# Performance work log

Hardware: AMD Instinct MI355X
Metric: run time of the kernel (lower is better)

The kernel has to match this reference:

```python
import jax, jax.numpy as jnp
import numpy as np

NUM_LAYERS = 4
D_MODEL = 512
D_INNER = 1024   # 2 * d_model (Mamba expand=2)
D_STATE = 16
DT_RANK = 32     # ceil(d_model / 16)
D_CONV = 4
BATCH = 2
SEQ = 512
EPS = 1e-5


def _rmsnorm(x, w, eps=EPS):
    # fused add+RMSNorm math: fp32 reduction, scale by weight (no bias)
    x = x.astype(jnp.float32)
    return x * jax.lax.rsqrt(jnp.mean(x * x, axis=-1, keepdims=True) + eps) * w


def _silu(x):
    return x * jax.nn.sigmoid(x)


def _causal_conv(x, w, b):
    # x: (B, D, L); w: (D, K) depthwise causal conv, left-pad K-1, take first L
    xp = jnp.pad(x, ((0, 0), (0, 0), (D_CONV - 1, 0)))
    out = jax.lax.conv_general_dilated(
        xp, w[:, None, :], (1,), 'VALID',
        dimension_numbers=('NCH', 'OIH', 'NCH'),
        feature_group_count=x.shape[1])
    return out + b[None, :, None]


def _selective_scan(u, delta, A, Bm, Cm):
    # u, delta: (B, D, L); A: (D, N); Bm, Cm: (B, N, L)
    xs = (jnp.moveaxis(delta, 2, 0), jnp.moveaxis(u, 2, 0),
          jnp.moveaxis(Bm, 2, 0), jnp.moveaxis(Cm, 2, 0))
    h0 = jnp.zeros((u.shape[0], u.shape[1], A.shape[1]), u.dtype)

    def step(h, xst):
        d_t, u_t, b_t, c_t = xst                     # (B,D),(B,D),(B,N),(B,N)
        dA = jnp.exp(d_t[:, :, None] * A[None])      # (B,D,N) ZOH discretization
        h = h * dA + (d_t * u_t)[:, :, None] * b_t[:, None, :]
        y = jnp.einsum('bdn,bn->bd', h, c_t)
        return h, y

    _, ys = jax.lax.scan(step, h0, xs)
    return jnp.moveaxis(ys, 0, 2)                    # (B, D, L)


def _ssm_branch(x, z, cw, cb, xpw, dtw, dtb, Alog, Dskip):
    x = _silu(_causal_conv(x, cw, cb))                              # (B, Din, L)
    x_dbl = jnp.einsum('rd,bdl->brl', xpw, x)                       # (B, R+2N, L)
    dt, Bm, Cm = jnp.split(x_dbl, [DT_RANK, DT_RANK + D_STATE], axis=1)
    delta = jax.nn.softplus(jnp.einsum('dr,brl->bdl', dtw, dt) + dtb[None, :, None])
    A = -jnp.exp(Alog.astype(jnp.float32))                          # (Din, N)
    y = _selective_scan(x, delta, A, Bm, Cm)
    y = y + Dskip[None, :, None] * x
    return y * _silu(z)


def _encoder(x, norm_w, in_proj_w, convw_f, convb_f, xpw_f, dtw_f, dtb_f,
             Alog_f, Dskip_f, convw_r, convb_r, xpw_r, dtw_r, dtb_r,
             Alog_r, Dskip_r, out_proj_w, normf_w):
    residual = None
    hs = x
    feats = []
    for i in range(NUM_LAYERS):
        # fused add + RMSNorm, prenorm=True, residual_in_fp32
        residual = hs if residual is None else (hs + residual)
        residual = residual.astype(jnp.float32)
        hn = _rmsnorm(residual, norm_w[i])
        # bimamba v2 mixer
        xz = jnp.einsum('ed,bld->bel', in_proj_w[i], hn)            # (B, 2Din, L)
        xi, zi = jnp.split(xz, 2, axis=1)
        y_f = _ssm_branch(xi, zi, convw_f[i], convb_f[i], xpw_f[i], dtw_f[i],
                          dtb_f[i], Alog_f[i], Dskip_f[i])
        y_r = _ssm_branch(xi[:, :, ::-1], zi[:, :, ::-1], convw_r[i], convb_r[i],
                          xpw_r[i], dtw_r[i], dtb_r[i], Alog_r[i], Dskip_r[i])
        y = y_f + y_r[:, :, ::-1]
        hs = jnp.einsum('bel,de->bld', y, out_proj_w[i])
        feats.append(hs)
    out = _rmsnorm(hs + residual, normf_w)                          # prenorm=False
    return out, feats


def setup_inputs() -> dict:
    key = jax.random.key(0)
    ks = jax.random.split(key, 12)
    Ly = NUM_LAYERS
    s = 0.02

    def nrm(k, shape):
        return jax.random.normal(k, shape, jnp.float32) * s

    dt = 1e-3 + jax.random.uniform(ks[11], (Ly, D_INNER), jnp.float32) * (0.1 - 1e-3)
    dtb = jnp.log(jnp.expm1(dt))  # inverse softplus of dt init
    Alog = jnp.log(jnp.broadcast_to(
        jnp.arange(1, D_STATE + 1, dtype=jnp.float32), (Ly, D_INNER, D_STATE)))
    return dict(
        x=jax.random.normal(ks[0], (BATCH, SEQ, D_MODEL), jnp.float32),
        norm_w=jnp.ones((Ly, D_MODEL), jnp.float32),
        in_proj_w=nrm(ks[1], (Ly, 2 * D_INNER, D_MODEL)),
        convw_f=nrm(ks[2], (Ly, D_INNER, D_CONV)),
        convb_f=jnp.zeros((Ly, D_INNER), jnp.float32),
        xpw_f=nrm(ks[3], (Ly, DT_RANK + 2 * D_STATE, D_INNER)),
        dtw_f=nrm(ks[4], (Ly, D_INNER, DT_RANK)),
        dtb_f=dtb,
        Alog_f=Alog,
        Dskip_f=jnp.ones((Ly, D_INNER), jnp.float32),
        convw_r=nrm(ks[5], (Ly, D_INNER, D_CONV)),
        convb_r=jnp.zeros((Ly, D_INNER), jnp.float32),
        xpw_r=nrm(ks[6], (Ly, DT_RANK + 2 * D_STATE, D_INNER)),
        dtw_r=nrm(ks[7], (Ly, D_INNER, DT_RANK)),
        dtb_r=dtb,
        Alog_r=Alog,
        Dskip_r=jnp.ones((Ly, D_INNER), jnp.float32),
        out_proj_w=nrm(ks[8], (Ly, D_MODEL, D_INNER)),
        normf_w=jnp.ones((D_MODEL,), jnp.float32),
    )


def reference(x, norm_w, in_proj_w, convw_f, convb_f, xpw_f, dtw_f, dtb_f,
              Alog_f, Dskip_f, convw_r, convb_r, xpw_r, dtw_r, dtb_r,
              Alog_r, Dskip_r, out_proj_w, normf_w):
    out, feats = _encoder(x, norm_w, in_proj_w, convw_f, convb_f, xpw_f, dtw_f,
                          dtb_f, Alog_f, Dskip_f, convw_r, convb_r, xpw_r,
                          dtw_r, dtb_r, Alog_r, Dskip_r, out_proj_w, normf_w)
    return (out, jnp.stack(feats))
```

## Files before the change

kernel.cpp:

```cpp
#include <hip/hip_runtime.h>

#define BATCH 2
#define SEQ 512
#define DMODEL 512
#define DINNER 1024
#define DSTATE 16
#define DTRANK 32
#define NBL (BATCH*SEQ)
#define EPSV 1e-5f

typedef __attribute__((ext_vector_type(8))) short bf16x8;
typedef __attribute__((ext_vector_type(4))) float f32x4;

static __device__ __forceinline__ float sigmoidf_(float x) {
  return 1.0f / (1.0f + __expf(-x));
}
static __device__ __forceinline__ float softplusf_(float x) {
  return fmaxf(x, 0.0f) + log1pf(__expf(-fabsf(x)));
}
static __device__ __forceinline__ unsigned short f2bf(float x) {
  unsigned int u = __float_as_uint(x);
  unsigned int r = (u + 0x7FFFu + ((u >> 16) & 1u)) >> 16;
  return (unsigned short)r;
}

__global__ __launch_bounds__(256) void wconvert_kernel(
    const float* __restrict__ s0, const float* __restrict__ s1,
    const float* __restrict__ s2, const float* __restrict__ s3,
    const float* __restrict__ s4, const float* __restrict__ s5,
    unsigned short* __restrict__ d0, unsigned short* __restrict__ d1,
    unsigned short* __restrict__ d2, unsigned short* __restrict__ d3,
    unsigned short* __restrict__ d4, unsigned short* __restrict__ d5) {
  long i = (long)(blockIdx.x * 256 + threadIdx.x) * 8;
  const float* src; unsigned short* dst;
  if (i < 4194304)      { src = s0; dst = d0; }
  else if (i < 6291456) { src = s1; dst = d1; i -= 4194304; }
  else if (i < 6553600) { src = s2; dst = d2; i -= 6291456; }
  else if (i < 6815744) { src = s3; dst = d3; i -= 6553600; }
  else if (i < 6946816) { src = s4; dst = d4; i -= 6815744; }
  else                  { src = s5; dst = d5; i -= 6946816; }
  const float4 v0 = *(const float4*)&src[i];
  const float4 v1 = *(const float4*)&src[i + 4];
  bf16x8 o;
  o[0] = (short)f2bf(v0.x); o[1] = (short)f2bf(v0.y);
  o[2] = (short)f2bf(v0.z); o[3] = (short)f2bf(v0.w);
  o[4] = (short)f2bf(v1.x); o[5] = (short)f2bf(v1.y);
  o[6] = (short)f2bf(v1.z); o[7] = (short)f2bf(v1.w);
  *(bf16x8*)&dst[i] = o;
}

__global__ __launch_bounds__(256) void addnorm_kernel(
    const float* __restrict__ hs, float* __restrict__ residual,
    const float* __restrict__ w, float* __restrict__ out,
    unsigned short* __restrict__ outb, int first) {
  const int row = blockIdx.x;
  const int t = threadIdx.x;
  const float* hp = hs + (long)row * DMODEL;
  float* rp = residual + (long)row * DMODEL;
  float r0 = hp[t], r1 = hp[t + 256];
  if (!first) { r0 += rp[t]; r1 += rp[t + 256]; }
  rp[t] = r0; rp[t + 256] = r1;
  float ss = r0 * r0 + r1 * r1;
  #pragma unroll
  for (int off = 32; off; off >>= 1) ss += __shfl_xor(ss, off, 64);
  __shared__ float sw[4];
  const int wid = t >> 6, lane = t & 63;
  if (lane == 0) sw[wid] = ss;
  __syncthreads();
  const float tot = sw[0] + sw[1] + sw[2] + sw[3];
  const float scale = rsqrtf(tot * (1.0f / (float)DMODEL) + EPSV);
  const float v0 = r0 * scale * w[t];
  const float v1 = r1 * scale * w[t + 256];
  if (out) {
    out[(long)row * DMODEL + t] = v0;
    out[(long)row * DMODEL + t + 256] = v1;
  }
  if (outb) {
    outb[(long)row * DMODEL + t] = f2bf(v0);
    outb[(long)row * DMODEL + t + 256] = f2bf(v1);
  }
}

#define LDK 40
#define LDK2 72

__global__ __launch_bounds__(256) void gemm_in_kernel(
    const unsigned short* __restrict__ A, const unsigned short* __restrict__ B,
    float* __restrict__ C) {
  __shared__ unsigned short As[128 * LDK2];
  __shared__ unsigned short Bs[64 * LDK2];
  const int t = threadIdx.x;
  const int m0 = blockIdx.y * 128, n0 = blockIdx.x * 64;
  const int lane = t & 63;
  const int w = t >> 6;
  const int wr = (w >> 1) * 64, wc = (w & 1) * 32;
  const int fr = lane & 15;
  const int fq = lane >> 4;
  const int K = DMODEL;

  f32x4 acc[4][2];
  #pragma unroll
  for (int i = 0; i < 4; ++i)
    #pragma unroll
    for (int j = 0; j < 2; ++j) {
      f32x4 z = {0.f, 0.f, 0.f, 0.f};
      acc[i][j] = z;
    }

  const int arow = t >> 1, ako = (t & 1) * 32;
  const int brow = t >> 2, bko = (t & 3) * 16;

  bf16x8 pa[4], pb[2];
  #define LOADG_IN(k0_) do {                                              \
    const unsigned short* ap = &A[(long)(m0 + arow) * K + (k0_) + ako];   \
    pa[0] = *(const bf16x8*)ap;        pa[1] = *(const bf16x8*)(ap + 8);  \
    pa[2] = *(const bf16x8*)(ap + 16); pa[3] = *(const bf16x8*)(ap + 24); \
    const unsigned short* bp = &B[(long)(n0 + brow) * K + (k0_) + bko];   \
    pb[0] = *(const bf16x8*)bp;        pb[1] = *(const bf16x8*)(bp + 8);  \
  } while (0)

  LOADG_IN(0);
  for (int k0 = 0; k0 < K; k0 += 64) {
    if (k0) __syncthreads();
    *(bf16x8*)&As[arow * LDK2 + ako]      = pa[0];
    *(bf16x8*)&As[arow * LDK2 + ako + 8]  = pa[1];
    *(bf16x8*)&As[arow * LDK2 + ako + 16] = pa[2];
    *(bf16x8*)&As[arow * LDK2 + ako + 24] = pa[3];
    *(bf16x8*)&Bs[brow * LDK2 + bko]      = pb[0];
    *(bf16x8*)&Bs[brow * LDK2 + bko + 8]  = pb[1];
    __syncthreads();
    if (k0 + 64 < K) LOADG_IN(k0 + 64);
    #pragma unroll
    for (int h = 0; h < 2; ++h) {
      bf16x8 af[4], bg[2];
      #pragma unroll
      for (int i = 0; i < 4; ++i)
        af[i] = *(const bf16x8*)&As[(wr + i * 16 + fr) * LDK2 + h * 32 + fq * 8];
      #pragma unroll
      for (int j = 0; j < 2; ++j)
        bg[j] = *(const bf16x8*)&Bs[(wc + j * 16 + fr) * LDK2 + h * 32 + fq * 8];
      #pragma unroll
      for (int i = 0; i < 4; ++i)
        #pragma unroll
        for (int j = 0; j < 2; ++j)
          acc[i][j] = __builtin_amdgcn_mfma_f32_16x16x32_bf16(
              af[i], bg[j], acc[i][j], 0, 0, 0);
    }
  }
  #undef LOADG_IN

  #pragma unroll
  for (int i = 0; i < 4; ++i)
    #pragma unroll
    for (int j = 0; j < 2; ++j)
      #pragma unroll
      for (int r2 = 0; r2 < 4; ++r2) {
        const int m = m0 + wr + i * 16 + fq * 4 + r2;
        const int n = n0 + wc + j * 16 + fr;
        C[(long)m * NBL + n] = acc[i][j][r2];
      }
}

__global__ __launch_bounds__(256) void conv_silu_kernel(
    const float* __restrict__ xz,
    const float* __restrict__ cw_f, const float* __restrict__ cb_f,
    const float* __restrict__ cw_r, const float* __restrict__ cb_r,
    unsigned short* __restrict__ xcT) {
  __shared__ unsigned short tile[32][33];
  const int dir = blockIdx.z;
  const int n0 = blockIdx.x * 32, d0 = blockIdx.y * 32;
  const int b = n0 >> 9;
  const int l0 = n0 & (SEQ - 1);
  const float* cw = dir ? cw_r : cw_f;
  const float* cb = dir ? cb_r : cb_f;
  unsigned short* dst = xcT + (long)dir * DINNER * NBL;
  const int t = threadIdx.x;
  const int c = t & 31, rr = t >> 5;
  #pragma unroll
  for (int p = 0; p < 4; ++p) {
    const int d = d0 + p * 8 + rr;
    const int l = l0 + c;
    const float* xi = xz + (long)d * NBL + b * SEQ;
    float sum = cb[d];
    #pragma unroll
    for (int k = 0; k < 4; ++k) {
      const int tt = l - 3 + k;
      if (tt >= 0) {
        const int src = dir ? (SEQ - 1 - tt) : tt;
        sum += cw[d * 4 + k] * xi[src];
      }
    }
    const float v = sum * sigmoidf_(sum);
    tile[p * 8 + rr][c] = f2bf(v);
  }
  __syncthreads();
  #pragma unroll
  for (int p = 0; p < 4; ++p) {
    const int n = n0 + p * 8 + rr;
    dst[(long)n * DINNER + d0 + c] = tile[c][p * 8 + rr];
  }
}

__global__ __launch_bounds__(256) void xdbl_mfma_kernel(
    const unsigned short* __restrict__ xpwb_f, const unsigned short* __restrict__ xpwb_r,
    const unsigned short* __restrict__ xcT,
    unsigned short* __restrict__ dtT,
    float* __restrict__ xbc_f, float* __restrict__ xbc_r) {
  __shared__ unsigned short As[64 * LDK2];
  __shared__ unsigned short Bs[32 * LDK2];
  const int t = threadIdx.x;
  const int dir = blockIdx.y;
  const int n0 = blockIdx.x * 32;
  const unsigned short* A = dir ? xpwb_r : xpwb_f;
  const unsigned short* B = xcT + (long)dir * DINNER * NBL;
  float* xbc = dir ? xbc_r : xbc_f;
  unsigned short* dtt = dtT + (long)dir * NBL * DTRANK;

  const int lane = t & 63;
  const int w = t >> 6;
  const int wr = (w >> 1) * 32, wc = (w & 1) * 16;
  const int fr = lane & 15;
  const int fq = lane >> 4;

  f32x4 acc[2];
  #pragma unroll
  for (int i = 0; i < 2; ++i) {
    f32x4 z = {0.f, 0.f, 0.f, 0.f};
    acc[i] = z;
  }

  const int arow = t >> 2, ako = (t & 3) * 16;
  const int brow = t >> 3, bko = (t & 7) * 8;

  bf16x8 pa[2], pb;
  #define LOADG_XD(k0_) do {                                                   \
    const unsigned short* ap = &A[(long)arow * DINNER + (k0_) + ako];          \
    pa[0] = *(const bf16x8*)ap;        pa[1] = *(const bf16x8*)(ap + 8);       \
    pb = *(const bf16x8*)&B[(long)(n0 + brow) * DINNER + (k0_) + bko];         \
  } while (0)

  LOADG_XD(0);
  for (int k0 = 0; k0 < DINNER; k0 += 64) {
    if (k0) __syncthreads();
    *(bf16x8*)&As[arow * LDK2 + ako]     = pa[0];
    *(bf16x8*)&As[arow * LDK2 + ako + 8] = pa[1];
    *(bf16x8*)&Bs[brow * LDK2 + bko]     = pb;
    __syncthreads();
    if (k0 + 64 < DINNER) LOADG_XD(k0 + 64);
    #pragma unroll
    for (int h = 0; h < 2; ++h) {
      bf16x8 af[2], bg;
      #pragma unroll
      for (int i = 0; i < 2; ++i)
        af[i] = *(const bf16x8*)&As[(wr + i * 16 + fr) * LDK2 + h * 32 + fq * 8];
      bg = *(const bf16x8*)&Bs[(wc + fr) * LDK2 + h * 32 + fq * 8];
      #pragma unroll
      for (int i = 0; i < 2; ++i)
        acc[i] = __builtin_amdgcn_mfma_f32_16x16x32_bf16(af[i], bg, acc[i], 0, 0, 0);
    }
  }
  #undef LOADG_XD

  #pragma unroll
  for (int i = 0; i < 2; ++i)
    #pragma unroll
    for (int r2 = 0; r2 < 4; ++r2) {
      const int m = wr + i * 16 + fq * 4 + r2;
      const int n = n0 + wc + fr;
      const float v = acc[i][r2];
      if (m < DTRANK) dtt[(long)n * DTRANK + m] = f2bf(v);
      else xbc[(long)(m - 32) * NBL + n] = v;
    }
}

__global__ __launch_bounds__(256) void deltam_kernel(
    const unsigned short* __restrict__ dtwb_f, const unsigned short* __restrict__ dtwb_r,
    const unsigned short* __restrict__ dtT,
    const float* __restrict__ dtb_f, const float* __restrict__ dtb_r,
    float* __restrict__ delta_f, float* __restrict__ delta_r) {
  __shared__ unsigned short As[128 * LDK];
  __shared__ unsigned short Bs[128 * LDK];
  const int t = threadIdx.x;
  const int dir = blockIdx.z;
  const unsigned short* A = dir ? dtwb_r : dtwb_f;
  const unsigned short* B = dtT + (long)dir * NBL * DTRANK;
  const float* dtb = dir ? dtb_r : dtb_f;
  float* dl = dir ? delta_r : delta_f;
  const int m0 = blockIdx.y * 128, n0 = blockIdx.x * 128;
  const int lane = t & 63;
  const int w = t >> 6;
  const int wr = (w >> 1) * 64, wc = (w & 1) * 64;
  const int fr = lane & 15;
  const int fq = lane >> 4;

  const int srow = t >> 1;
  const int sko = (t & 1) * 16;
  *(bf16x8*)&As[srow * LDK + sko] =
      *(const bf16x8*)&A[(long)(m0 + srow) * DTRANK + sko];
  *(bf16x8*)&As[srow * LDK + sko + 8] =
      *(const bf16x8*)&A[(long)(m0 + srow) * DTRANK + sko + 8];
  *(bf16x8*)&Bs[srow * LDK + sko] =
      *(const bf16x8*)&B[(long)(n0 + srow) * DTRANK + sko];
  *(bf16x8*)&Bs[srow * LDK + sko + 8] =
      *(const bf16x8*)&B[(long)(n0 + srow) * DTRANK + sko + 8];
  __syncthreads();

  bf16x8 af[4], bg[4];
  #pragma unroll
  for (int i = 0; i < 4; ++i) {
    af[i] = *(const bf16x8*)&As[(wr + i * 16 + fr) * LDK + fq * 8];
    bg[i] = *(const bf16x8*)&Bs[(wc + i * 16 + fr) * LDK + fq * 8];
  }
  f32x4 acc[4][4];
  #pragma unroll
  for (int i = 0; i < 4; ++i)
    #pragma unroll
    for (int j = 0; j < 4; ++j) {
      f32x4 z = {0.f, 0.f, 0.f, 0.f};
      acc[i][j] = __builtin_amdgcn_mfma_f32_16x16x32_bf16(af[i], bg[j], z, 0, 0, 0);
    }

  #pragma unroll
  for (int i = 0; i < 4; ++i) {
    const int m = m0 + wr + i * 16 + fq * 4;
    #pragma unroll
    for (int r2 = 0; r2 < 4; ++r2) {
      const float bias = dtb[m + r2];
      #pragma unroll
      for (int j = 0; j < 4; ++j) {
        const int n = n0 + wc + j * 16 + fr;
        dl[(long)(m + r2) * NBL + n] = softplusf_(acc[i][j][r2] + bias);
      }
    }
  }
}

static __device__ __forceinline__ void scan_pass(
    const float* __restrict__ dp, const float u[8],
    const float* __restrict__ bct, const float* __restrict__ Alog,
    float Dv, int lane, float out[8]) {
  float dt[8], dtu[8];
  {
    const float4 a0 = *(const float4*)&dp[0];
    const float4 a1 = *(const float4*)&dp[4];
    dt[0] = a0.x; dt[1] = a0.y; dt[2] = a0.z; dt[3] = a0.w;
    dt[4] = a1.x; dt[5] = a1.y; dt[6] = a1.z; dt[7] = a1.w;
  }
  #pragma unroll
  for (int j = 0; j < 8; ++j) { dtu[j] = dt[j] * u[j]; out[j] = 0.f; }

  for (int n = 0; n < DSTATE; ++n) {
    const float An = -__expf(Alog[n]);
    float Bv[8], Cv[8], dA[8], cB[8];
    {
      const float* bp = bct + (long)n * NBL;
      const float* cp = bct + (long)(DSTATE + n) * NBL;
      const float4 b0 = *(const float4*)&bp[0];
      const float4 b1 = *(const float4*)&bp[4];
      Bv[0] = b0.x; Bv[1] = b0.y; Bv[2] = b0.z; Bv[3] = b0.w;
      Bv[4] = b1.x; Bv[5] = b1.y; Bv[6] = b1.z; Bv[7] = b1.w;
      const float4 c0 = *(const float4*)&cp[0];
      const float4 c1 = *(const float4*)&cp[4];
      Cv[0] = c0.x; Cv[1] = c0.y; Cv[2] = c0.z; Cv[3] = c0.w;
      Cv[4] = c1.x; Cv[5] = c1.y; Cv[6] = c1.z; Cv[7] = c1.w;
    }
    float h = 0.f, P = 1.f;
    #pragma unroll
    for (int j = 0; j < 8; ++j) {
      dA[j] = __expf(dt[j] * An);
      cB[j] = dtu[j] * Bv[j];
      h = fmaf(h, dA[j], cB[j]);
      P *= dA[j];
    }
    float hs = h, Ps = P;
    #pragma unroll
    for (int off = 1; off < 64; off <<= 1) {
      const float hp = __shfl_up(hs, off, 64);
      const float Pp = __shfl_up(Ps, off, 64);
      if (lane >= off) { hs = fmaf(hp, Ps, hs); Ps *= Pp; }
    }
    float h0 = __shfl_up(hs, 1, 64);
    if (lane == 0) h0 = 0.f;
    #pragma unroll
    for (int j = 0; j < 8; ++j) {
      h0 = fmaf(h0, dA[j], cB[j]);
      out[j] = fmaf(h0, Cv[j], out[j]);
    }
  }
  #pragma unroll
  for (int j = 0; j < 8; ++j) out[j] = fmaf(Dv, u[j], out[j]);
}

__global__ __launch_bounds__(512) void scan_split_kernel(
    const float* __restrict__ delta_f, const float* __restrict__ delta_r,
    const float* __restrict__ xbc_f, const float* __restrict__ xbc_r,
    const float* __restrict__ Alog_f, const float* __restrict__ Alog_r,
    const float* __restrict__ Dsk_f, const float* __restrict__ Dsk_r,
    const float* __restrict__ cw_f, const float* __restrict__ cb_f,
    const float* __restrict__ cw_r, const float* __restrict__ cb_r,
    const float* __restrict__ xz, unsigned short* __restrict__ ybt) {
  __shared__ float s_r[4][512];
  __shared__ unsigned short s_y[4][512];
  const int t = threadIdx.x;
  const int wv = t >> 6;
  const int lane = t & 63;
  const int dir = wv & 1;
  const int dl = wv >> 1;
  const int row = blockIdx.x * 4 + dl;
  const int b = row >> 10, d = row & 1023;
  const long rbase = (long)d * NBL + b * SEQ;

  float xv[8];
  {
    const float* xp = xz + rbase + lane * 8;
    const float4 a0 = *(const float4*)&xp[0];
    const float4 a1 = *(const float4*)&xp[4];
    xv[0] = a0.x; xv[1] = a0.y; xv[2] = a0.z; xv[3] = a0.w;
    xv[4] = a1.x; xv[5] = a1.y; xv[6] = a1.z; xv[7] = a1.w;
  }
  if (dir) {
    float xr[8];
    #pragma unroll
    for (int j = 0; j < 8; ++j) xr[j] = __shfl(xv[7 - j], 63 - lane, 64);
    #pragma unroll
    for (int j = 0; j < 8; ++j) xv[j] = xr[j];
  }
  const float* cwp = dir ? cw_r : cw_f;
  const float* cbp = dir ? cb_r : cb_f;
  float u[8];
  {
    const float cw0 = cwp[d * 4], cw1 = cwp[d * 4 + 1], cw2 = cwp[d * 4 + 2],
                cw3 = cwp[d * 4 + 3], cb = cbp[d];
    const float xm1 = __shfl_up(xv[7], 1, 64);
    const float xm2 = __shfl_up(xv[6], 1, 64);
    const float xm3 = __shfl_up(xv[5], 1, 64);
    const float ext[3] = {xm3, xm2, xm1};
    #pragma unroll
    for (int j = 0; j < 8; ++j) {
      float s = cb + cw3 * xv[j];
      const int p = lane * 8 + j;
      #pragma unroll
      for (int k = 0; k < 3; ++k) {
        const int idx = j - 3 + k;
        const float xval = (idx >= 0) ? xv[idx] : ext[3 + idx];
        if (p - 3 + k >= 0) s += (k == 0 ? cw0 : (k == 1 ? cw1 : cw2)) * xval;
      }
      u[j] = s * sigmoidf_(s);
    }
  }

  float a[8];
  scan_pass((dir ? delta_r : delta_f) + rbase + lane * 8, u,
            (dir ? xbc_r : xbc_f) + b * SEQ + lane * 8,
            (dir ? Alog_r : Alog_f) + d * DSTATE,
            (dir ? Dsk_r : Dsk_f)[d], lane, a);

  if (dir) {
    #pragma unroll
    for (int j = 0; j < 8; ++j) {
      const float v = __shfl(a[7 - j], 63 - lane, 64);
      s_r[dl][lane * 8 + j] = v;
    }
  }
  __syncthreads();
  if (!dir) {
    const float* zp = xz + (long)(DINNER + d) * NBL + b * SEQ + lane * 8;
    const float4 z0 = *(const float4*)&zp[0];
    const float4 z1 = *(const float4*)&zp[4];
    const float zv[8] = {z0.x, z0.y, z0.z, z0.w, z1.x, z1.y, z1.z, z1.w};
    #pragma unroll
    for (int j = 0; j < 8; ++j) {
      const float tot = a[j] + s_r[dl][lane * 8 + j];
      s_y[dl][lane * 8 + j] = f2bf(tot * (zv[j] * sigmoidf_(zv[j])));
    }
  }
  __syncthreads();
  const int d0 = (blockIdx.x * 4) & 1023;
  const int bb = (blockIdx.x * 4) >> 10;
  unsigned short* yrow = ybt + (long)(bb * SEQ) * DINNER + d0;
  {
    const int n = t;
    ushort4 v = {s_y[0][n], s_y[1][n], s_y[2][n], s_y[3][n]};
    *(ushort4*)&yrow[(long)n * DINNER] = v;
  }
}

__global__ __launch_bounds__(256) void gemm_out_kernel(
    const unsigned short* __restrict__ A, const unsigned short* __restrict__ B,
    float* __restrict__ C) {
  __shared__ unsigned short As[64 * LDK2];
  __shared__ unsigned short Bs[64 * LDK2];
  const int t = threadIdx.x;
  const int m0 = blockIdx.y * 64, n0 = blockIdx.x * 64;
  const int lane = t & 63;
  const int w = t >> 6;
  const int wr = (w >> 1) * 32, wc = (w & 1) * 32;
  const int fr = lane & 15;
  const int fq = lane >> 4;
  const int K = DINNER;

  f32x4 acc[2][2];
  #pragma unroll
  for (int i = 0; i < 2; ++i)
    #pragma unroll
    for (int j = 0; j < 2; ++j) {
      f32x4 z = {0.f, 0.f, 0.f, 0.f};
      acc[i][j] = z;
    }

  const int arow = t >> 2, ako = (t & 3) * 16;

  bf16x8 pa[2], pb[2];
  #define LOADG_OUT(k0_) do {                                              \
    const unsigned short* ap = &A[(long)(m0 + arow) * K + (k0_) + ako];    \
    pa[0] = *(const bf16x8*)ap;        pa[1] = *(const bf16x8*)(ap + 8);   \
    const unsigned short* bp = &B[(long)(n0 + arow) * K + (k0_) + ako];    \
    pb[0] = *(const bf16x8*)bp;        pb[1] = *(const bf16x8*)(bp + 8);   \
  } while (0)

  LOADG_OUT(0);
  for (int k0 = 0; k0 < K; k0 += 64) {
    if (k0) __syncthreads();
    *(bf16x8*)&As[arow * LDK2 + ako]     = pa[0];
    *(bf16x8*)&As[arow * LDK2 + ako + 8] = pa[1];
    *(bf16x8*)&Bs[arow * LDK2 + ako]     = pb[0];
    *(bf16x8*)&Bs[arow * LDK2 + ako + 8] = pb[1];
    __syncthreads();
    if (k0 + 64 < K) LOADG_OUT(k0 + 64);
    #pragma unroll
    for (int h = 0; h < 2; ++h) {
      bf16x8 af[2], bg[2];
      #pragma unroll
      for (int i = 0; i < 2; ++i) {
        af[i] = *(const bf16x8*)&As[(wr + i * 16 + fr) * LDK2 + h * 32 + fq * 8];
        bg[i] = *(const bf16x8*)&Bs[(wc + i * 16 + fr) * LDK2 + h * 32 + fq * 8];
      }
      #pragma unroll
      for (int i = 0; i < 2; ++i)
        #pragma unroll
        for (int j = 0; j < 2; ++j)
          acc[i][j] = __builtin_amdgcn_mfma_f32_16x16x32_bf16(
              af[i], bg[j], acc[i][j], 0, 0, 0);
    }
  }
  #undef LOADG_OUT

  #pragma unroll
  for (int i = 0; i < 2; ++i)
    #pragma unroll
    for (int j = 0; j < 2; ++j)
      #pragma unroll
      for (int r2 = 0; r2 < 4; ++r2) {
        const int m = m0 + wr + i * 16 + fq * 4 + r2;
        const int n = n0 + wc + j * 16 + fr;
        C[(long)n * DMODEL + m] = acc[i][j][r2];
      }
}

extern "C" void kernel_launch(void* const* d_in, const int* in_sizes, int n_in,
                              void* d_out, int out_size, void* d_ws, size_t ws_size,
                              hipStream_t stream) {
  (void)in_sizes; (void)n_in; (void)out_size; (void)ws_size;
  const float* x       = (const float*)d_in[0];
  const float* norm_w  = (const float*)d_in[1];
  const float* in_proj = (const float*)d_in[2];
  const float* convw_f = (const float*)d_in[3];
  const float* convb_f = (const float*)d_in[4];
  const float* xpw_f   = (const float*)d_in[5];
  const float* dtw_f   = (const float*)d_in[6];
  const float* dtb_f   = (const float*)d_in[7];
  const float* Alog_f  = (const float*)d_in[8];
  const float* Dsk_f   = (const float*)d_in[9];
  const float* convw_r = (const float*)d_in[10];
  const float* convb_r = (const float*)d_in[11];
  const float* xpw_r   = (const float*)d_in[12];
  const float* dtw_r   = (const float*)d_in[13];
  const float* dtb_r   = (const float*)d_in[14];
  const float* Alog_r  = (const float*)d_in[15];
  const float* Dsk_r   = (const float*)d_in[16];
  const float* out_w   = (const float*)d_in[17];
  const float* normf_w = (const float*)d_in[18];

  float* ws = (float*)d_ws;
  float* residual = ws;  ws += 524288;
  float* xzbuf    = ws;  ws += 2097152;
  float* xbc_f    = ws;  ws += 32768;
  float* xbc_r    = ws;  ws += 32768;
  float* delta_f  = ws;  ws += 1048576;
  float* delta_r  = ws;  ws += 1048576;
  float* hnb_f    = ws;  ws += 262144;
  float* wbfin_f  = ws;  ws += 2097152;
  float* wbfout_f = ws;  ws += 1048576;
  float* ybt_f    = ws;  ws += 524288;
  float* xcT_f    = ws;  ws += 1048576;
  float* dtT_f    = ws;  ws += 32768;
  float* xpwb_f_  = ws;  ws += 131072;
  float* xpwb_r_  = ws;  ws += 131072;
  float* dtwb_f_  = ws;  ws += 65536;
  float* dtwb_r_  = ws;  ws += 65536;

  unsigned short* hnb = (unsigned short*)hnb_f;
  unsigned short* wbfin = (unsigned short*)wbfin_f;
  unsigned short* wbfout = (unsigned short*)wbfout_f;
  unsigned short* ybt = (unsigned short*)ybt_f;
  unsigned short* xcT = (unsigned short*)xcT_f;
  unsigned short* dtT = (unsigned short*)dtT_f;
  unsigned short* xpwb_f = (unsigned short*)xpwb_f_;
  unsigned short* xpwb_r = (unsigned short*)xpwb_r_;
  unsigned short* dtwb_f = (unsigned short*)dtwb_f_;
  unsigned short* dtwb_r = (unsigned short*)dtwb_r_;

  float* outp = (float*)d_out;

  wconvert_kernel<<<3456, 256, 0, stream>>>(
      in_proj, out_w, xpw_f, xpw_r, dtw_f, dtw_r,
      wbfin, wbfout, xpwb_f, xpwb_r, dtwb_f, dtwb_r);

  for (int layer = 0; layer < 4; ++layer) {
    const float* hsrc = layer == 0 ? x : (outp + (long)layer * 524288);
    addnorm_kernel<<<1024, 256, 0, stream>>>(
        hsrc, residual, norm_w + layer * DMODEL, nullptr, hnb, layer == 0 ? 1 : 0);
    gemm_in_kernel<<<dim3(16, 16), 256, 0, stream>>>(
        wbfin + (long)layer * 2048 * 512, hnb, xzbuf);
    conv_silu_kernel<<<dim3(32, 32, 2), 256, 0, stream>>>(
        xzbuf, convw_f + layer * DINNER * 4, convb_f + layer * DINNER,
        convw_r + layer * DINNER * 4, convb_r + layer * DINNER, xcT);
    xdbl_mfma_kernel<<<dim3(32, 2), 256, 0, stream>>>(
        xpwb_f + (long)layer * 64 * DINNER, xpwb_r + (long)layer * 64 * DINNER,
        xcT, dtT, xbc_f, xbc_r);
    deltam_kernel<<<dim3(8, 8, 2), 256, 0, stream>>>(
        dtwb_f + (long)layer * DINNER * DTRANK, dtwb_r + (long)layer * DINNER * DTRANK,
        dtT, dtb_f + layer * DINNER, dtb_r + layer * DINNER, delta_f, delta_r);
    scan_split_kernel<<<512, 512, 0, stream>>>(
        delta_f, delta_r, xbc_f, xbc_r,
        Alog_f + layer * DINNER * DSTATE, Alog_r + layer * DINNER * DSTATE,
        Dsk_f + layer * DINNER, Dsk_r + layer * DINNER,
        convw_f + layer * DINNER * 4, convb_f + layer * DINNER,
        convw_r + layer * DINNER * 4, convb_r + layer * DINNER,
        xzbuf, ybt);
    gemm_out_kernel<<<dim3(16, 8), 256, 0, stream>>>(
        wbfout + (long)layer * 512 * 1024, ybt,
        outp + (long)(1 + layer) * 524288);
  }
  addnorm_kernel<<<1024, 256, 0, stream>>>(
      outp + 4 * 524288, residual, normf_w, outp, nullptr, 0);
}
```

Baseline: 328.3 us.

## Fuse delta projection and softplus into the selective scan kernel

Removes the separate MFMA-based delta kernel and instead computes each channel's delta inside the scan kernel as a 32-wide dot product of the bf16 dt_proj row with the bf16 dt features, followed by softplus. This drops one launch per layer and the write and read of two 4 MB fp32 delta buffers. The cost is scalar FMAs per thread (32 per timestep) instead of matrix-core work, plus redundant reads of dtT across the channels of a block. It also vectorizes the reverse-direction shared-memory exchange and the bf16 output store.

```diff
diff --git a/kernel.cpp b/kernel.cpp
--- a/kernel.cpp
+++ b/kernel.cpp
@@ -22,6 +22,9 @@
   unsigned int u = __float_as_uint(x);
   unsigned int r = (u + 0x7FFFu + ((u >> 16) & 1u)) >> 16;
   return (unsigned short)r;
+}
+static __device__ __forceinline__ float bf2f(short s) {
+  return __uint_as_float(((unsigned int)(unsigned short)s) << 16);
 }
 
 __global__ __launch_bounds__(256) void wconvert_kernel(
@@ -81,7 +84,6 @@
   }
 }
 
-#define LDK 40
 #define LDK2 72
 
 __global__ __launch_bounds__(256) void gemm_in_kernel(
@@ -273,79 +275,11 @@
     }
 }
 
-__global__ __launch_bounds__(256) void deltam_kernel(
-    const unsigned short* __restrict__ dtwb_f, const unsigned short* __restrict__ dtwb_r,
-    const unsigned short* __restrict__ dtT,
-    const float* __restrict__ dtb_f, const float* __restrict__ dtb_r,
-    float* __restrict__ delta_f, float* __restrict__ delta_r) {
-  __shared__ unsigned short As[128 * LDK];
-  __shared__ unsigned short Bs[128 * LDK];
-  const int t = threadIdx.x;
-  const int dir = blockIdx.z;
-  const unsigned short* A = dir ? dtwb_r : dtwb_f;
-  const unsigned short* B = dtT + (long)dir * NBL * DTRANK;
-  const float* dtb = dir ? dtb_r : dtb_f;
-  float* dl = dir ? delta_r : delta_f;
-  const int m0 = blockIdx.y * 128, n0 = blockIdx.x * 128;
-  const int lane = t & 63;
-  const int w = t >> 6;
-  const int wr = (w >> 1) * 64, wc = (w & 1) * 64;
-  const int fr = lane & 15;
-  const int fq = lane >> 4;
-
-  const int srow = t >> 1;
-  const int sko = (t & 1) * 16;
-  *(bf16x8*)&As[srow * LDK + sko] =
-      *(const bf16x8*)&A[(long)(m0 + srow) * DTRANK + sko];
-  *(bf16x8*)&As[srow * LDK + sko + 8] =
-      *(const bf16x8*)&A[(long)(m0 + srow) * DTRANK + sko + 8];
-  *(bf16x8*)&Bs[srow * LDK + sko] =
-      *(const bf16x8*)&B[(long)(n0 + srow) * DTRANK + sko];
-  *(bf16x8*)&Bs[srow * LDK + sko + 8] =
-      *(const bf16x8*)&B[(long)(n0 + srow) * DTRANK + sko + 8];
-  __syncthreads();
-
-  bf16x8 af[4], bg[4];
-  #pragma unroll
-  for (int i = 0; i < 4; ++i) {
-    af[i] = *(const bf16x8*)&As[(wr + i * 16 + fr) * LDK + fq * 8];
-    bg[i] = *(const bf16x8*)&Bs[(wc + i * 16 + fr) * LDK + fq * 8];
-  }
-  f32x4 acc[4][4];
-  #pragma unroll
-  for (int i = 0; i < 4; ++i)
-    #pragma unroll
-    for (int j = 0; j < 4; ++j) {
-      f32x4 z = {0.f, 0.f, 0.f, 0.f};
-      acc[i][j] = __builtin_amdgcn_mfma_f32_16x16x32_bf16(af[i], bg[j], z, 0, 0, 0);
-    }
-
-  #pragma unroll
-  for (int i = 0; i < 4; ++i) {
-    const int m = m0 + wr + i * 16 + fq * 4;
-    #pragma unroll
-    for (int r2 = 0; r2 < 4; ++r2) {
-      const float bias = dtb[m + r2];
-      #pragma unroll
-      for (int j = 0; j < 4; ++j) {
-        const int n = n0 + wc + j * 16 + fr;
-        dl[(long)(m + r2) * NBL + n] = softplusf_(acc[i][j][r2] + bias);
-      }
-    }
-  }
-}
-
 static __device__ __forceinline__ void scan_pass(
-    const float* __restrict__ dp, const float u[8],
+    const float dt[8], const float u[8],
     const float* __restrict__ bct, const float* __restrict__ Alog,
     float Dv, int lane, float out[8]) {
-  float dt[8], dtu[8];
-  {
-    const float4 a0 = *(const float4*)&dp[0];
-    const float4 a1 = *(const float4*)&dp[4];
-    dt[0] = a0.x; dt[1] = a0.y; dt[2] = a0.z; dt[3] = a0.w;
-    dt[4] = a1.x; dt[5] = a1.y; dt[6] = a1.z; dt[7] = a1.w;
-  }
+  float dtu[8];
   #pragma unroll
   for (int j = 0; j < 8; ++j) { dtu[j] = dt[j] * u[j]; out[j] = 0.f; }
 
@@ -392,14 +326,16 @@
 }
 
 __global__ __launch_bounds__(512) void scan_split_kernel(
-    const float* __restrict__ delta_f, const float* __restrict__ delta_r,
+    const unsigned short* __restrict__ dtT,
+    const unsigned short* __restrict__ dtwb_f, const unsigned short* __restrict__ dtwb_r,
+    const float* __restrict__ dtb_f, const float* __restrict__ dtb_r,
     const float* __restrict__ xbc_f, const float* __restrict__ xbc_r,
     const float* __restrict__ Alog_f, const float* __restrict__ Alog_r,
     const float* __restrict__ Dsk_f, const float* __restrict__ Dsk_r,
     const float* __restrict__ cw_f, const float* __restrict__ cb_f,
     const float* __restrict__ cw_r, const float* __restrict__ cb_r,
     const float* __restrict__ xz, unsigned short* __restrict__ ybt) {
-  __shared__ float s_r[4][512];
+  __shared__ float s_r[4][2][256];
   __shared__ unsigned short s_y[4][512];
   const int t = threadIdx.x;
   const int wv = t >> 6;
@@ -449,18 +385,48 @@
     }
   }
 
+  float dtv[8];
+  {
+    const unsigned short* dw = ((dir ? dtwb_r : dtwb_f)) + (long)d * DTRANK;
+    float w32[32];
+    #pragma unroll
+    for (int q = 0; q < 4; ++q) {
+      const bf16x8 v = *(const bf16x8*)&dw[q * 8];
+      #pragma unroll
+      for (int e = 0; e < 8; ++e) w32[q * 8 + e] = bf2f(v[e]);
+    }
+    const float bias = (dir ? dtb_r : dtb_f)[d];
+    const unsigned short* dtrow =
+        dtT + (long)dir * NBL * DTRANK + ((long)b * SEQ + lane * 8) * DTRANK;
+    #pragma unroll
+    for (int j = 0; j < 8; ++j) {
+      const bf16x8* rp = (const bf16x8*)&dtrow[(long)j * DTRANK];
+      float acc = bias;
+      #pragma unroll
+      for (int q = 0; q < 4; ++q) {
+        const bf16x8 rv = rp[q];
+        #pragma unroll
+        for (int e = 0; e < 8; ++e)
+          acc = fmaf(w32[q * 8 + e], bf2f(rv[e]), acc);
+      }
+      dtv[j] = softplusf_(acc);
+    }
+  }
+
   float a[8];
-  scan_pass((dir ? delta_r : delta_f) + rbase + lane * 8, u,
+  scan_pass(dtv, u,
             (dir ? xbc_r : xbc_f) + b * SEQ + lane * 8,
             (dir ? Alog_r : Alog_f) + d * DSTATE,
             (dir ? Dsk_r : Dsk_f)[d], lane, a);
 
   if (dir) {
-    #pragma unroll
-    for (int j = 0; j < 8; ++j) {
-      const float v = __shfl(a[7 - j], 63 - lane, 64);
-      s_r[dl][lane * 8 + j] = v;
-    }
+    float fv[8];
+    #pragma unroll
+    for (int j = 0; j < 8; ++j) fv[j] = __shfl(a[7 - j], 63 - lane, 64);
+    float4 q0 = {fv[0], fv[1], fv[2], fv[3]};
+    float4 q1 = {fv[4], fv[5], fv[6], fv[7]};
+    *(float4*)&s_r[dl][0][lane * 4] = q0;
+    *(float4*)&s_r[dl][1][lane * 4] = q1;
   }
   __syncthreads();
   if (!dir) {
@@ -468,11 +434,16 @@
     const float4 z0 = *(const float4*)&zp[0];
     const float4 z1 = *(const float4*)&zp[4];
     const float zv[8] = {z0.x, z0.y, z0.z, z0.w, z1.x, z1.y, z1.z, z1.w};
+    const float4 r0 = *(const float4*)&s_r[dl][0][lane * 4];
+    const float4 r1 = *(const float4*)&s_r[dl][1][lane * 4];
+    const float rr[8] = {r0.x, r0.y, r0.z, r0.w, r1.x, r1.y, r1.z, r1.w};
+    bf16x8 ob;
     #pragma unroll
     for (int j = 0; j < 8; ++j) {
-      const float tot = a[j] + s_r[dl][lane * 8 + j];
-      s_y[dl][lane * 8 + j] = f2bf(tot * (zv[j] * sigmoidf_(zv[j])));
-    }
+      const float tot = a[j] + rr[j];
+      ob[j] = (short)f2bf(tot * (zv[j] * sigmoidf_(zv[j])));
+    }
+    *(bf16x8*)&s_y[dl][lane * 8] = ob;
   }
   __syncthreads();
   const int d0 = (blockIdx.x * 4) & 1023;
@@ -586,8 +557,6 @@
   float* xzbuf    = ws;  ws += 2097152;
   float* xbc_f    = ws;  ws += 32768;
   float* xbc_r    = ws;  ws += 32768;
-  float* delta_f  = ws;  ws += 1048576;
-  float* delta_r  = ws;  ws += 1048576;
   float* hnb_f    = ws;  ws += 262144;
   float* wbfin_f  = ws;  ws += 2097152;
   float* wbfout_f = ws;  ws += 1048576;
@@ -628,11 +597,11 @@
     xdbl_mfma_kernel<<<dim3(32, 2), 256, 0, stream>>>(
         xpwb_f + (long)layer * 64 * DINNER, xpwb_r + (long)layer * 64 * DINNER,
         xcT, dtT, xbc_f, xbc_r);
-    deltam_kernel<<<dim3(8, 8, 2), 256, 0, stream>>>(
-        dtwb_f + (long)layer * DINNER * DTRANK, dtwb_r + (long)layer * DINNER * DTRANK,
-        dtT, dtb_f + layer * DINNER, dtb_r + layer * DINNER, delta_f, delta_r);
     scan_split_kernel<<<512, 512, 0, stream>>>(
-        delta_f, delta_r, xbc_f, xbc_r,
+        dtT, dtwb_f + (long)layer * DINNER * DTRANK,
+        dtwb_r + (long)layer * DINNER * DTRANK,
+        dtb_f + layer * DINNER, dtb_r + layer * DINNER,
+        xbc_f, xbc_r,
         Alog_f + layer * DINNER * DSTATE, Alog_r + layer * DINNER * DSTATE,
         Dsk_f + layer * DINNER, Dsk_r + layer * DINNER,
         convw_f + layer * DINNER * 4, convb_f + layer * DINNER,
```

Result: faster. 316.9 us (median of 2 runs) (-3.5%).
